# Kernel optimization log

Hardware: AMD Instinct MI355X
Metric: run time of the kernel (lower is better)

## Reference

```python
import jax, jax.numpy as jnp
import numpy as np

THRESH_FACTOR = 0.7


def ternarize(w):
    # w: [in_features, out_features]; per-row (dim 0) delta/alpha stats
    n = w.shape[1]
    abs_w = jnp.abs(w)
    delta = (THRESH_FACTOR / n) * abs_w.sum(axis=1, keepdims=True)  # [in, 1]
    mask = abs_w > delta
    count = mask.sum(axis=1, keepdims=True).astype(w.dtype)
    alpha = jnp.where(mask, abs_w, 0).sum(axis=1, keepdims=True) / count  # [in, 1]
    tern = jnp.where(w > delta, 1.0, jnp.where(w < -delta, -1.0, 0.0)).astype(w.dtype)
    return tern * alpha


def setup_inputs() -> dict:
    key = jax.random.key(0)
    k1, k2, k3 = jax.random.split(key, 3)
    B, IN, OUT = 8192, 4096, 4096
    x = jax.random.normal(k1, (B, IN), dtype=jnp.float32)
    # kaiming-uniform-ish then clamp to [-1, 1] as in the module
    bound_w = float(np.sqrt(6.0 / ((1.0 + 5.0) * IN)))
    weights = jax.random.uniform(k2, (IN, OUT), minval=-bound_w, maxval=bound_w, dtype=jnp.float32)
    weights = jnp.clip(weights, -1.0, 1.0)
    bound_b = 1.0 / float(np.sqrt(IN))
    bias = jax.random.uniform(k3, (OUT,), minval=-bound_b, maxval=bound_b, dtype=jnp.float32)
    return {"x": x, "weights": weights, "bias": bias}


def reference(x, weights, bias):
    w_t = ternarize(weights)
    return jnp.matmul(x, w_t) + bias
```

## Files before the change

kernel.cpp:

```cpp
#include <hip/hip_runtime.h>
#include <stdint.h>
#include <stddef.h>

#define IN_F 4096
#define OUT_F 4096

typedef int i32x4 __attribute__((ext_vector_type(4)));


__device__ static inline void async16(const void* g, void* l) {
    __builtin_amdgcn_global_load_lds(
        (const __attribute__((address_space(1))) unsigned int*)g,
        (__attribute__((address_space(3))) unsigned int*)l,
        16, 0, 0);
}

__device__ static inline double wred_d(double v) {
#pragma unroll
    for (int o = 32; o > 0; o >>= 1) v += __shfl_down(v, o, 64);
    return v;
}

__device__ static inline int wred_i(int v) {
#pragma unroll
    for (int o = 32; o > 0; o >>= 1) v += __shfl_down(v, o, 64);
    return v;
}

__device__ static inline float wred_max(float v) {
#pragma unroll
    for (int o = 32; o > 0; o >>= 1) v = fmaxf(v, __shfl_down(v, o, 64));
    return v;
}


__global__ __launch_bounds__(256) void rowstats_kernel(
    const float* __restrict__ w,
    float* __restrict__ alpha_o,
    double* __restrict__ delta_o) {
    __shared__ double sh_s[4], sh_m[4];
    __shared__ int sh_c[4];
    const int row = blockIdx.x;
    const int t = threadIdx.x;
    const int lane = t & 63, wv = t >> 6;
    const float4* wr = (const float4*)(w + (size_t)row * OUT_F + t * 16);

    float4 v[4];
    double s = 0.0;
#pragma unroll
    for (int i = 0; i < 4; ++i) {
        v[i] = wr[i];
        s += (double)fabsf(v[i].x) + (double)fabsf(v[i].y) +
             (double)fabsf(v[i].z) + (double)fabsf(v[i].w);
    }
    double sw = wred_d(s);
    if (lane == 0) sh_s[wv] = sw;
    __syncthreads();
    const double delta = (sh_s[0] + sh_s[1] + sh_s[2] + sh_s[3]) *
                         (0.7 / (double)OUT_F);

    double ms = 0.0;
    int cnt = 0;
#pragma unroll
    for (int i = 0; i < 4; ++i) {
        float f[4] = {v[i].x, v[i].y, v[i].z, v[i].w};
#pragma unroll
        for (int j = 0; j < 4; ++j) {
            double a = (double)fabsf(f[j]);
            if (a > delta) { ms += a; ++cnt; }
        }
    }
    double msw = wred_d(ms);
    int cw = wred_i(cnt);
    if (lane == 0) { sh_m[wv] = msw; sh_c[wv] = cw; }
    __syncthreads();
    if (t == 0) {
        double mtot = sh_m[0] + sh_m[1] + sh_m[2] + sh_m[3];
        int ctot = sh_c[0] + sh_c[1] + sh_c[2] + sh_c[3];
        alpha_o[row] = (float)(mtot / (double)ctot);
        delta_o[row] = delta;
    }
}


__global__ __launch_bounds__(256) void tern_transpose_kernel(
    const float* __restrict__ w,
    const double* __restrict__ delta_i,
    int8_t* __restrict__ Tt) {
    __shared__ unsigned int ldsb[128 * 33];
    const int t = threadIdx.x;
    const int i0 = blockIdx.y * 128;
    const int j0 = blockIdx.x * 128;

#pragma unroll
    for (int it = 0; it < 4; ++it) {
        int bb = it * 256 + t;
        int rg = bb >> 5;
        int cc = bb & 31;
        unsigned int col[4] = {0u, 0u, 0u, 0u};
#pragma unroll
        for (int k = 0; k < 4; ++k) {
            int irow = i0 + rg * 4 + k;
            float4 v = *(const float4*)(w + (size_t)irow * OUT_F + j0 + cc * 4);
            double d = delta_i[irow];
            float f[4] = {v.x, v.y, v.z, v.w};
#pragma unroll
            for (int j = 0; j < 4; ++j) {
                int q = ((double)f[j] > d) ? 1 : (((double)f[j] < -d) ? -1 : 0);
                col[j] |= (unsigned int)(q & 0xff) << (k * 8);
            }
        }
#pragma unroll
        for (int j = 0; j < 4; ++j)
            ldsb[(cc * 4 + j) * 33 + rg] = col[j];
    }
    __syncthreads();
#pragma unroll
    for (int it = 0; it < 4; ++it) {
        int idx = it * 256 + t;
        int rr = idx >> 3;
        int c2 = idx & 7;
        uint4 o;
        o.x = ldsb[rr * 33 + c2 * 4 + 0];
        o.y = ldsb[rr * 33 + c2 * 4 + 1];
        o.z = ldsb[rr * 33 + c2 * 4 + 2];
        o.w = ldsb[rr * 33 + c2 * 4 + 3];
        *(uint4*)(Tt + (size_t)(j0 + rr) * IN_F + i0 + c2 * 16) = o;
    }
}


__global__ __launch_bounds__(256) void xquant_kernel(
    const float* __restrict__ x,
    const float* __restrict__ alpha,
    int8_t* __restrict__ xq,
    float* __restrict__ scale_o) {
    __shared__ float sh_mx[4];
    const int row = blockIdx.x;
    const int t = threadIdx.x;
    const int lane = t & 63, wv = t >> 6;
    const float4* xr = (const float4*)(x + (size_t)row * IN_F + t * 16);
    const float4* ar = (const float4*)(alpha + t * 16);

    float4 xs[4];
    float mx = 0.0f;
#pragma unroll
    for (int i = 0; i < 4; ++i) {
        float4 v = xr[i];
        float4 a = ar[i];
        v.x *= a.x; v.y *= a.y; v.z *= a.z; v.w *= a.w;
        xs[i] = v;
        mx = fmaxf(mx, fmaxf(fmaxf(fabsf(v.x), fabsf(v.y)),
                             fmaxf(fabsf(v.z), fabsf(v.w))));
    }
    float mw = wred_max(mx);
    if (lane == 0) sh_mx[wv] = mw;
    __syncthreads();
    const float rmax = fmaxf(fmaxf(sh_mx[0], sh_mx[1]), fmaxf(sh_mx[2], sh_mx[3]));
    const float inv = (rmax > 0.0f) ? (127.0f / rmax) : 0.0f;

    uint4 o;
    unsigned int* op = (unsigned int*)&o;
#pragma unroll
    for (int i = 0; i < 4; ++i) {
        float f[4] = {xs[i].x, xs[i].y, xs[i].z, xs[i].w};
        unsigned int d = 0;
#pragma unroll
        for (int j = 0; j < 4; ++j) {
            int q = __float2int_rn(f[j] * inv);
            d |= (unsigned int)(q & 0xff) << (j * 8);
        }
        op[i] = d;
    }
    *(uint4*)(xq + (size_t)row * IN_F + t * 16) = o;
    if (t == 0) scale_o[row] = (rmax > 0.0f) ? (rmax / 127.0f) : 1.0f;
}


#define GBARRIER() asm volatile("s_barrier" ::: "memory")

#define STAGE(G, GR0, TILE, LBASE, HALF)                                        \
    do {                                                                        \
        _Pragma("unroll")                                                       \
        for (int rr_ = 0; rr_ < 2; ++rr_) {                                     \
            const int L_ = (HALF) * 1024 + rr_ * 512 + t;                       \
            const int row_ = L_ >> 3;                                           \
            const int gch_ = (L_ & 7) ^ (row_ & 7);                             \
            async16((G) + (size_t)((GR0) + row_) * IN_F + (TILE) * 128 +        \
                        (gch_ << 4),                                            \
                    (LBASE) + (L_ << 4));                                       \
        }                                                                       \
    } while (0)

#define READ_A(BUF, MI0)                                                        \
    _Pragma("unroll")                                                           \
    for (int mi_ = 0; mi_ < 4; ++mi_) {                                         \
        a[2 * mi_]     = *(const i32x4*)((BUF) + offA_k0 + ((MI0) + mi_) * 2048); \
        a[2 * mi_ + 1] = *(const i32x4*)((BUF) + offA_k1 + ((MI0) + mi_) * 2048); \
    }

#define READ_B(BUF, NI0, DST)                                                   \
    _Pragma("unroll")                                                           \
    for (int ni_ = 0; ni_ < 2; ++ni_) {                                         \
        DST[2 * ni_]     = *(const i32x4*)((BUF) + offB_k0 + ((NI0) + ni_) * 2048); \
        DST[2 * ni_ + 1] = *(const i32x4*)((BUF) + offB_k1 + ((NI0) + ni_) * 2048); \
    }

#define MFMA_Q(MI0, NI0, BSRC)                                                  \
    do {                                                                        \
        __builtin_amdgcn_s_setprio(1);                                          \
        _Pragma("unroll")                                                       \
        for (int mi_ = 0; mi_ < 4; ++mi_) {                                     \
            _Pragma("unroll")                                                   \
            for (int ni_ = 0; ni_ < 2; ++ni_) {                                 \
                acc[(MI0) + mi_][(NI0) + ni_] =                                 \
                    __builtin_amdgcn_mfma_i32_16x16x64_i8(                      \
                        a[2 * mi_], BSRC[2 * ni_],                              \
                        acc[(MI0) + mi_][(NI0) + ni_], 0, 0, 0);                \
                acc[(MI0) + mi_][(NI0) + ni_] =                                 \
                    __builtin_amdgcn_mfma_i32_16x16x64_i8(                      \
                        a[2 * mi_ + 1], BSRC[2 * ni_ + 1],                      \
                        acc[(MI0) + mi_][(NI0) + ni_], 0, 0, 0);                \
            }                                                                   \
        }                                                                       \
        __builtin_amdgcn_s_setprio(0);                                          \
    } while (0)

__global__ __launch_bounds__(512, 2) void gemm_i8_8ph(
    const int8_t* __restrict__ Xq,
    const int8_t* __restrict__ Tq,
    const float* __restrict__ scale,
    const float* __restrict__ bias,
    float* __restrict__ out) {
    extern __shared__ __align__(16) int8_t lds[];
    const int K = IN_F;
    const int NT = K / 128;
    const int NI = NT / 2;

    const int t = threadIdx.x;
    const int lane = t & 63;
    const int wave = t >> 6;
    const int lm = lane & 15;
    const int qh = lane >> 4;
    const int wm = (wave >> 2) << 7;
    const int wn = (wave & 3) << 6;

    const int nwg = gridDim.x;
    const int id = blockIdx.x;
    const int swz = (id & 7) * (nwg >> 3) + (id >> 3);
    const int m0 = (swz >> 4) << 8;
    const int n0 = (swz & 15) << 8;

    int8_t* const A0  = lds;
    int8_t* const B0  = lds + 32768;
    int8_t* const A1b = lds + 65536;
    int8_t* const B1b = lds + 98304;

    const int swzs = lm & 7;
    const int offA_k0 = (wm + lm) * 128 + ((qh ^ swzs) << 4);
    const int offA_k1 = (wm + lm) * 128 + (((4 + qh) ^ swzs) << 4);
    const int offB_k0 = (wn + lm) * 128 + ((qh ^ swzs) << 4);
    const int offB_k1 = (wn + lm) * 128 + (((4 + qh) ^ swzs) << 4);

    i32x4 acc[8][4];
#pragma unroll
    for (int i = 0; i < 8; ++i)
#pragma unroll
        for (int j = 0; j < 4; ++j)
#pragma unroll
            for (int r = 0; r < 4; ++r) acc[i][j][r] = 0;

    i32x4 a[8], bA[4], bB[4];

    STAGE(Xq, m0, 0, A0, 0);
    STAGE(Xq, m0, 0, A0, 1);
    STAGE(Tq, n0, 0, B0, 0);
    STAGE(Tq, n0, 0, B0, 1);
    STAGE(Tq, n0, 1, B1b, 0);
    STAGE(Xq, m0, 1, A1b, 0);
    asm volatile("s_waitcnt vmcnt(4)" ::: "memory");
    GBARRIER();

#pragma unroll 1
    for (int i = 0; i < NI; ++i) {
        const int kt = 2 * i;
        READ_A(A0, 0);
        READ_B(B0, 0, bA);
        STAGE(Tq, n0, kt + 1, B1b, 1);
        GBARRIER();
        MFMA_Q(0, 0, bA);
        GBARRIER();
        READ_B(B0, 2, bB);
        STAGE(Xq, m0, kt + 1, A1b, 1);
        GBARRIER();
        MFMA_Q(0, 2, bB);
        GBARRIER();
        READ_A(A0, 4);
        if (kt + 2 < NT) STAGE(Tq, n0, kt + 2, B0, 0);
        GBARRIER();
        MFMA_Q(4, 0, bA);
        GBARRIER();
        if (kt + 2 < NT) STAGE(Xq, m0, kt + 2, A0, 0);
        GBARRIER();
        MFMA_Q(4, 2, bB);
        if (i + 1 < NI) asm volatile("s_waitcnt vmcnt(4)" ::: "memory");
        else            asm volatile("s_waitcnt vmcnt(0)" ::: "memory");
        GBARRIER();
        READ_A(A1b, 0);
        READ_B(B1b, 0, bA);
        if (kt + 2 < NT) STAGE(Tq, n0, kt + 2, B0, 1);
        GBARRIER();
        MFMA_Q(0, 0, bA);
        GBARRIER();
        READ_B(B1b, 2, bB);
        if (kt + 2 < NT) STAGE(Xq, m0, kt + 2, A0, 1);
        GBARRIER();
        MFMA_Q(0, 2, bB);
        GBARRIER();
        READ_A(A1b, 4);
        if (kt + 3 < NT) STAGE(Tq, n0, kt + 3, B1b, 0);
        GBARRIER();
        MFMA_Q(4, 0, bA);
        GBARRIER();
        if (kt + 3 < NT) STAGE(Xq, m0, kt + 3, A1b, 0);
        GBARRIER();
        MFMA_Q(4, 2, bB);
        if (i + 1 < NI) asm volatile("s_waitcnt vmcnt(4)" ::: "memory");
        GBARRIER();
    }

    const int q4 = qh << 2;
#pragma unroll
    for (int mi = 0; mi < 8; ++mi) {
        float sc[4];
#pragma unroll
        for (int r = 0; r < 4; ++r) sc[r] = scale[m0 + wm + mi * 16 + q4 + r];
#pragma unroll
        for (int ni = 0; ni < 4; ++ni) {
            int col = n0 + wn + ni * 16 + lm;
            float b = bias[col];
#pragma unroll
            for (int r = 0; r < 4; ++r) {
                int row = m0 + wm + mi * 16 + q4 + r;
                out[(size_t)row * OUT_F + col] =
                    (float)acc[mi][ni][r] * sc[r] + b;
            }
        }
    }
}


extern "C" void kernel_launch(void* const* d_in, const int* in_sizes, int n_in,
                              void* d_out, int out_size, void* d_ws, size_t ws_size,
                              hipStream_t stream) {
    const float* x = (const float*)d_in[0];
    const float* w = (const float*)d_in[1];
    const float* bias = (const float*)d_in[2];
    float* out = (float*)d_out;
    const int B = in_sizes[0] / IN_F;

    char* ws = (char*)d_ws;
    int8_t* Tt = (int8_t*)ws;
    int8_t* Xq = (int8_t*)(ws + (size_t)16777216);
    float* alpha = (float*)(ws + (size_t)50331648);
    double* delta = (double*)(ws + (size_t)50331648 + 16384);
    float* scale = (float*)(ws + (size_t)50331648 + 16384);

    static int lds_set = 0;
    if (!lds_set) {
        hipFuncSetAttribute((const void*)gemm_i8_8ph,
                            hipFuncAttributeMaxDynamicSharedMemorySize, 131072);
        lds_set = 1;
    }

    rowstats_kernel<<<IN_F, 256, 0, stream>>>(w, alpha, delta);
    tern_transpose_kernel<<<dim3(OUT_F / 128, IN_F / 128), 256, 0, stream>>>(w, delta, Tt);
    xquant_kernel<<<B, 256, 0, stream>>>(x, alpha, Xq, scale);
    const int nwg = (B / 256) * (OUT_F / 256);
    gemm_i8_8ph<<<dim3(nwg), dim3(512), 131072, stream>>>(Xq, Tt, scale, bias, out);
}
```

Measured before the change: 390.9 us.

## Fuse ternarization into row stats and restructure GEMM main-loop staging

The row-stats kernel now emits packed int8 ternary values directly, so the transpose kernel only shuffles bytes and no longer rereads the fp32 weights or a per-row double delta. Prep kernels switch to coalesced strided float4 access. The GEMM main loop is rescheduled to issue whole A/B tile stages together and to batch LDS reads before pairs of MFMA groups, which cuts the number of workgroup barriers per iteration. The revised vmcnt waits and barrier placement could expose load latency or race on LDS buffers if the ordering assumptions are wrong.

```diff
diff --git a/kernel.cpp b/kernel.cpp
--- a/kernel.cpp
+++ b/kernel.cpp
@@ -34,24 +34,24 @@
 }
 
 
-__global__ __launch_bounds__(256) void rowstats_kernel(
+__global__ __launch_bounds__(256) void rowstats_tern_kernel(
     const float* __restrict__ w,
     float* __restrict__ alpha_o,
-    double* __restrict__ delta_o) {
+    unsigned int* __restrict__ Tp) {
     __shared__ double sh_s[4], sh_m[4];
     __shared__ int sh_c[4];
     const int row = blockIdx.x;
     const int t = threadIdx.x;
     const int lane = t & 63, wv = t >> 6;
-    const float4* wr = (const float4*)(w + (size_t)row * OUT_F + t * 16);
+    const float4* wr = (const float4*)(w + (size_t)row * OUT_F);
 
     float4 v[4];
     double s = 0.0;
 #pragma unroll
-    for (int i = 0; i < 4; ++i) {
-        v[i] = wr[i];
-        s += (double)fabsf(v[i].x) + (double)fabsf(v[i].y) +
-             (double)fabsf(v[i].z) + (double)fabsf(v[i].w);
+    for (int it = 0; it < 4; ++it) {
+        v[it] = wr[t + it * 256];
+        s += (double)fabsf(v[it].x) + (double)fabsf(v[it].y) +
+             (double)fabsf(v[it].z) + (double)fabsf(v[it].w);
     }
     double sw = wred_d(s);
     if (lane == 0) sh_s[wv] = sw;
@@ -59,16 +59,22 @@
     const double delta = (sh_s[0] + sh_s[1] + sh_s[2] + sh_s[3]) *
                          (0.7 / (double)OUT_F);
 
+    unsigned int* trow = Tp + (size_t)row * (OUT_F / 4);
     double ms = 0.0;
     int cnt = 0;
 #pragma unroll
-    for (int i = 0; i < 4; ++i) {
-        float f[4] = {v[i].x, v[i].y, v[i].z, v[i].w};
+    for (int it = 0; it < 4; ++it) {
+        float f[4] = {v[it].x, v[it].y, v[it].z, v[it].w};
+        unsigned int u = 0;
 #pragma unroll
         for (int j = 0; j < 4; ++j) {
             double a = (double)fabsf(f[j]);
             if (a > delta) { ms += a; ++cnt; }
-        }
+            int q = ((double)f[j] > delta) ? 1 :
+                    (((double)f[j] < -delta) ? -1 : 0);
+            u |= (unsigned int)(q & 0xff) << (j * 8);
+        }
+        trow[t + it * 256] = u;
     }
     double msw = wred_d(ms);
     int cw = wred_i(cnt);
@@ -78,14 +84,12 @@
         double mtot = sh_m[0] + sh_m[1] + sh_m[2] + sh_m[3];
         int ctot = sh_c[0] + sh_c[1] + sh_c[2] + sh_c[3];
         alpha_o[row] = (float)(mtot / (double)ctot);
-        delta_o[row] = delta;
-    }
-}
-
-
-__global__ __launch_bounds__(256) void tern_transpose_kernel(
-    const float* __restrict__ w,
-    const double* __restrict__ delta_i,
+    }
+}
+
+
+__global__ __launch_bounds__(256) void transpose_i8_kernel(
+    const unsigned int* __restrict__ Tp,
     int8_t* __restrict__ Tt) {
     __shared__ unsigned int ldsb[128 * 33];
     const int t = threadIdx.x;
@@ -100,15 +104,12 @@
         unsigned int col[4] = {0u, 0u, 0u, 0u};
 #pragma unroll
         for (int k = 0; k < 4; ++k) {
-            int irow = i0 + rg * 4 + k;
-            float4 v = *(const float4*)(w + (size_t)irow * OUT_F + j0 + cc * 4);
-            double d = delta_i[irow];
-            float f[4] = {v.x, v.y, v.z, v.w};
-#pragma unroll
-            for (int j = 0; j < 4; ++j) {
-                int q = ((double)f[j] > d) ? 1 : (((double)f[j] < -d) ? -1 : 0);
-                col[j] |= (unsigned int)(q & 0xff) << (k * 8);
-            }
+            unsigned int d = Tp[(size_t)(i0 + rg * 4 + k) * (OUT_F / 4) +
+                                (j0 >> 2) + cc];
+            col[0] |= (d & 0xffu) << (k * 8);
+            col[1] |= ((d >> 8) & 0xffu) << (k * 8);
+            col[2] |= ((d >> 16) & 0xffu) << (k * 8);
+            col[3] |= ((d >> 24) & 0xffu) << (k * 8);
         }
 #pragma unroll
         for (int j = 0; j < 4; ++j)
@@ -139,17 +140,17 @@
     const int row = blockIdx.x;
     const int t = threadIdx.x;
     const int lane = t & 63, wv = t >> 6;
-    const float4* xr = (const float4*)(x + (size_t)row * IN_F + t * 16);
-    const float4* ar = (const float4*)(alpha + t * 16);
+    const float4* xr = (const float4*)(x + (size_t)row * IN_F);
+    const float4* ar = (const float4*)alpha;
 
     float4 xs[4];
     float mx = 0.0f;
 #pragma unroll
-    for (int i = 0; i < 4; ++i) {
-        float4 v = xr[i];
-        float4 a = ar[i];
+    for (int it = 0; it < 4; ++it) {
+        float4 v = xr[t + it * 256];
+        float4 a = ar[t + it * 256];
         v.x *= a.x; v.y *= a.y; v.z *= a.z; v.w *= a.w;
-        xs[i] = v;
+        xs[it] = v;
         mx = fmaxf(mx, fmaxf(fmaxf(fabsf(v.x), fabsf(v.y)),
                              fmaxf(fabsf(v.z), fabsf(v.w))));
     }
@@ -159,20 +160,18 @@
     const float rmax = fmaxf(fmaxf(sh_mx[0], sh_mx[1]), fmaxf(sh_mx[2], sh_mx[3]));
     const float inv = (rmax > 0.0f) ? (127.0f / rmax) : 0.0f;
 
-    uint4 o;
-    unsigned int* op = (unsigned int*)&o;
-#pragma unroll
-    for (int i = 0; i < 4; ++i) {
-        float f[4] = {xs[i].x, xs[i].y, xs[i].z, xs[i].w};
-        unsigned int d = 0;
+    unsigned int* qd = (unsigned int*)(xq + (size_t)row * IN_F);
+#pragma unroll
+    for (int it = 0; it < 4; ++it) {
+        float f[4] = {xs[it].x, xs[it].y, xs[it].z, xs[it].w};
+        unsigned int u = 0;
 #pragma unroll
         for (int j = 0; j < 4; ++j) {
             int q = __float2int_rn(f[j] * inv);
-            d |= (unsigned int)(q & 0xff) << (j * 8);
-        }
-        op[i] = d;
-    }
-    *(uint4*)(xq + (size_t)row * IN_F + t * 16) = o;
+            u |= (unsigned int)(q & 0xff) << (j * 8);
+        }
+        qd[t + it * 256] = u;
+    }
     if (t == 0) scale_o[row] = (rmax > 0.0f) ? (rmax / 127.0f) : 1.0f;
 }
 
@@ -277,7 +276,7 @@
     STAGE(Tq, n0, 0, B0, 0);
     STAGE(Tq, n0, 0, B0, 1);
     STAGE(Tq, n0, 1, B1b, 0);
-    STAGE(Xq, m0, 1, A1b, 0);
+    STAGE(Tq, n0, 1, B1b, 1);
     asm volatile("s_waitcnt vmcnt(4)" ::: "memory");
     GBARRIER();
 
@@ -286,46 +285,44 @@
         const int kt = 2 * i;
         READ_A(A0, 0);
         READ_B(B0, 0, bA);
-        STAGE(Tq, n0, kt + 1, B1b, 1);
+        READ_B(B0, 2, bB);
+        STAGE(Xq, m0, kt + 1, A1b, 0);
+        STAGE(Xq, m0, kt + 1, A1b, 1);
         GBARRIER();
         MFMA_Q(0, 0, bA);
-        GBARRIER();
-        READ_B(B0, 2, bB);
-        STAGE(Xq, m0, kt + 1, A1b, 1);
-        GBARRIER();
         MFMA_Q(0, 2, bB);
         GBARRIER();
         READ_A(A0, 4);
-        if (kt + 2 < NT) STAGE(Tq, n0, kt + 2, B0, 0);
+        if (kt + 2 < NT) {
+            STAGE(Tq, n0, kt + 2, B0, 0);
+            STAGE(Tq, n0, kt + 2, B0, 1);
+        }
         GBARRIER();
         MFMA_Q(4, 0, bA);
-        GBARRIER();
-        if (kt + 2 < NT) STAGE(Xq, m0, kt + 2, A0, 0);
-        GBARRIER();
+        MFMA_Q(4, 2, bB);
+        asm volatile("s_waitcnt vmcnt(4)" ::: "memory");
+        GBARRIER();
+        READ_A(A1b, 0);
+        READ_B(B1b, 0, bA);
+        READ_B(B1b, 2, bB);
+        if (kt + 2 < NT) {
+            STAGE(Xq, m0, kt + 2, A0, 0);
+            STAGE(Xq, m0, kt + 2, A0, 1);
+        }
+        GBARRIER();
+        MFMA_Q(0, 0, bA);
+        MFMA_Q(0, 2, bB);
+        GBARRIER();
+        READ_A(A1b, 4);
+        if (kt + 3 < NT) {
+            STAGE(Tq, n0, kt + 3, B1b, 0);
+            STAGE(Tq, n0, kt + 3, B1b, 1);
+        }
+        GBARRIER();
+        MFMA_Q(4, 0, bA);
         MFMA_Q(4, 2, bB);
         if (i + 1 < NI) asm volatile("s_waitcnt vmcnt(4)" ::: "memory");
         else            asm volatile("s_waitcnt vmcnt(0)" ::: "memory");
-        GBARRIER();
-        READ_A(A1b, 0);
-        READ_B(B1b, 0, bA);
-        if (kt + 2 < NT) STAGE(Tq, n0, kt + 2, B0, 1);
-        GBARRIER();
-        MFMA_Q(0, 0, bA);
-        GBARRIER();
-        READ_B(B1b, 2, bB);
-        if (kt + 2 < NT) STAGE(Xq, m0, kt + 2, A0, 1);
-        GBARRIER();
-        MFMA_Q(0, 2, bB);
-        GBARRIER();
-        READ_A(A1b, 4);
-        if (kt + 3 < NT) STAGE(Tq, n0, kt + 3, B1b, 0);
-        GBARRIER();
-        MFMA_Q(4, 0, bA);
-        GBARRIER();
-        if (kt + 3 < NT) STAGE(Xq, m0, kt + 3, A1b, 0);
-        GBARRIER();
-        MFMA_Q(4, 2, bB);
-        if (i + 1 < NI) asm volatile("s_waitcnt vmcnt(4)" ::: "memory");
         GBARRIER();
     }
 
@@ -361,9 +358,9 @@
 
     char* ws = (char*)d_ws;
     int8_t* Tt = (int8_t*)ws;
+    unsigned int* Tp = (unsigned int*)(ws + (size_t)16777216);
     int8_t* Xq = (int8_t*)(ws + (size_t)16777216);
     float* alpha = (float*)(ws + (size_t)50331648);
-    double* delta = (double*)(ws + (size_t)50331648 + 16384);
     float* scale = (float*)(ws + (size_t)50331648 + 16384);
 
     static int lds_set = 0;
@@ -373,8 +370,8 @@
         lds_set = 1;
     }
 
-    rowstats_kernel<<<IN_F, 256, 0, stream>>>(w, alpha, delta);
-    tern_transpose_kernel<<<dim3(OUT_F / 128, IN_F / 128), 256, 0, stream>>>(w, delta, Tt);
+    rowstats_tern_kernel<<<IN_F, 256, 0, stream>>>(w, alpha, Tp);
+    transpose_i8_kernel<<<dim3(OUT_F / 128, IN_F / 128), 256, 0, stream>>>(Tp, Tt);
     xquant_kernel<<<B, 256, 0, stream>>>(x, alpha, Xq, scale);
     const int nwg = (B / 256) * (OUT_F / 256);
     gemm_i8_8ph<<<dim3(nwg), dim3(512), 131072, stream>>>(Xq, Tt, scale, bias, out);
```

Measured after the change: 385.2 us. No clear change (-1.4%).
